# Performance work log

Measured on AMD Instinct MI355X. Metric: run time of the kernel, lower is better.

Reference implementation:

```python
import jax, jax.numpy as jnp
import numpy as np

B, S, D, H = 4, 2048, 1024, 16
HD = D // H
DFF = 4 * D
NUM_LAYERS = 12
RES = 1.0 / float(np.sqrt(NUM_LAYERS))
SCALE = 1.0 / float(np.sqrt(D))  # module divides by sqrt(embed_dim), not head_dim
EPS = 1e-5


def setup_inputs() -> dict:
    key = jax.random.key(0)
    ks = jax.random.split(key, 12)
    s = 0.02
    p = lambda k, shp: (jax.random.normal(k, shp, jnp.float32) * s)
    return {
        "x": jax.random.normal(ks[0], (B, S, D), jnp.float32),
        "Wq": p(ks[1], (D, D)), "bq": jnp.zeros((D,), jnp.float32),
        "Wk": p(ks[2], (D, D)), "bk": jnp.zeros((D,), jnp.float32),
        "Wv": p(ks[3], (D, D)), "bv": jnp.zeros((D,), jnp.float32),
        "Wo": p(ks[4], (D, D)), "bo": jnp.zeros((D,), jnp.float32),
        "g1": jnp.ones((D,), jnp.float32), "be1": jnp.zeros((D,), jnp.float32),
        "g2": jnp.ones((D,), jnp.float32), "be2": jnp.zeros((D,), jnp.float32),
        "W1": p(ks[5], (D, DFF)), "b1": jnp.zeros((DFF,), jnp.float32),
        "W2": p(ks[6], (DFF, D)), "b2": jnp.zeros((D,), jnp.float32),
    }


def _layernorm(x, g, b):
    m = jnp.mean(x, axis=-1, keepdims=True)
    v = jnp.mean((x - m) ** 2, axis=-1, keepdims=True)
    return (x - m) * jax.lax.rsqrt(v + EPS) * g + b


def _attention(x, Wq, bq, Wk, bk, Wv, bv, Wo, bo):
    b, s, d = x.shape
    q = (x @ Wq + bq).reshape(b, s, H, HD)
    k = (x @ Wk + bk).reshape(b, s, H, HD)
    v = (x @ Wv + bv).reshape(b, s, H, HD)
    scores = jnp.einsum('bqhd,bkhd->bhqk', q, k) * SCALE  # [B,H,S,S]
    mask = jnp.tril(jnp.ones((s, s), dtype=bool))
    scores = jnp.where(mask, scores, -jnp.inf)
    attn = jax.nn.softmax(scores, axis=-1)  # dropout_rate=0 -> identity
    out = jnp.einsum('bhqk,bkhd->bqhd', attn, v).reshape(b, s, d)
    return out @ Wo + bo


def reference(x, Wq, bq, Wk, bk, Wv, bv, Wo, bo, g1, be1, g2, be2, W1, b1, W2, b2):
    x = x + RES * _attention(_layernorm(x, g1, be1), Wq, bq, Wk, bk, Wv, bv, Wo, bo)
    h = _layernorm(x, g2, be2)
    ffn = jax.nn.relu(h @ W1 + b1) @ W2 + b2
    x = x + RES * ffn
    return x
```

## Files before the change

kernel.cpp:

```cpp
#include <hip/hip_runtime.h>

typedef unsigned short ushort_t;
typedef unsigned int uint32;
typedef __attribute__((ext_vector_type(4))) float f32x4;
typedef __attribute__((ext_vector_type(8))) short bf16x8;

#define B_   4
#define S_   2048
#define D_   1024
#define H_   16
#define HD_  64
#define DFF_ 4096
#define M_   (B_ * S_)

#define RES_   0.28867513459481287f
#define SCALE_ 0.03125f
#define EPS_   1e-5f
#define LOG2E_ 1.4426950408889634f

__device__ __forceinline__ ushort_t f2bf(float f) {
    union { float f; uint32 u; } c; c.f = f;
    uint32 u = c.u + 0x7fffu + ((c.u >> 16) & 1u);
    return (ushort_t)(u >> 16);
}
__device__ __forceinline__ float bf2f(ushort_t h) {
    union { uint32 u; float f; } c; c.u = ((uint32)h) << 16;
    return c.f;
}
__device__ __forceinline__ float fexp2(float x) {
    float r; asm("v_exp_f32 %0, %1" : "=v"(r) : "v"(x)); return r;
}
__device__ __forceinline__ uint32 cvt_pk_bf16(float lo, float hi) {
    uint32 r;
    asm("v_cvt_pk_bf16_f32 %0, %1, %2" : "=v"(r) : "v"(lo), "v"(hi));
    return r;
}

#define GLDS(src_, dst_)                                                     \
    __builtin_amdgcn_global_load_lds(                                        \
        (const __attribute__((address_space(1))) void*)(src_),               \
        (__attribute__((address_space(3))) void*)(dst_), 16, 0, 0)

__global__ __launch_bounds__(256) void transpose_cast_kernel(
    const float* __restrict__ W, ushort_t* __restrict__ Wt, int K, int N)
{
    __shared__ float tile[32][33];
    const int bx = blockIdx.x * 32;
    const int by = blockIdx.y * 32;
    const int tx = threadIdx.x;
    const int ty = threadIdx.y;
    #pragma unroll
    for (int i = 0; i < 32; i += 8)
        tile[ty + i][tx] = W[(size_t)(by + ty + i) * N + bx + tx];
    __syncthreads();
    #pragma unroll
    for (int i = 0; i < 32; i += 8)
        Wt[(size_t)(bx + ty + i) * K + by + tx] = f2bf(tile[tx][ty + i]);
}

__global__ void concat_bias_kernel(const float* __restrict__ bq,
                                   const float* __restrict__ bk,
                                   const float* __restrict__ bv,
                                   float* __restrict__ bqkv)
{
    int i = blockIdx.x * blockDim.x + threadIdx.x;
    if (i < 3 * D_) {
        float v = (i < D_) ? bq[i] : (i < 2 * D_) ? bk[i - D_] : bv[i - 2 * D_];
        bqkv[i] = v;
    }
}

__global__ __launch_bounds__(256) void ln_kernel(
    const float* __restrict__ x, const float* __restrict__ g,
    const float* __restrict__ be, ushort_t* __restrict__ out)
{
    const int row = blockIdx.x;
    const int t = threadIdx.x;
    const int lane = t & 63;
    const int wave = t >> 6;
    const float4* xr = (const float4*)(x + (size_t)row * D_);
    float4 v = xr[t];
    float s  = v.x + v.y + v.z + v.w;
    float s2 = v.x * v.x + v.y * v.y + v.z * v.z + v.w * v.w;
    #pragma unroll
    for (int off = 32; off; off >>= 1) {
        s  += __shfl_xor(s, off);
        s2 += __shfl_xor(s2, off);
    }
    __shared__ float red[8];
    if (lane == 0) { red[wave * 2] = s; red[wave * 2 + 1] = s2; }
    __syncthreads();
    s  = red[0] + red[2] + red[4] + red[6];
    s2 = red[1] + red[3] + red[5] + red[7];
    const float mean = s * (1.0f / D_);
    const float var  = s2 * (1.0f / D_) - mean * mean;
    const float rstd = rsqrtf(var + EPS_);
    const float4 gv  = ((const float4*)g)[t];
    const float4 bv  = ((const float4*)be)[t];
    ushort_t o[4];
    o[0] = f2bf((v.x - mean) * rstd * gv.x + bv.x);
    o[1] = f2bf((v.y - mean) * rstd * gv.y + bv.y);
    o[2] = f2bf((v.z - mean) * rstd * gv.z + bv.z);
    o[3] = f2bf((v.w - mean) * rstd * gv.w + bv.w);
    *(ushort2*)&out[(size_t)row * D_ + t * 4]     = make_ushort2(o[0], o[1]);
    *(ushort2*)&out[(size_t)row * D_ + t * 4 + 2] = make_ushort2(o[2], o[3]);
}

__global__ __launch_bounds__(256) void vtrans_kernel(
    const ushort_t* __restrict__ qkv, ushort_t* __restrict__ vt)
{
    __shared__ __align__(16) ushort_t T[256 * 64];
    const int tid  = threadIdx.x;
    const int sblk = blockIdx.x & 7;
    const int bh   = blockIdx.x >> 3;
    const int b = bh >> 4, h = bh & 15;
    const ushort_t* src = qkv + (size_t)(b * S_ + sblk * 256) * (3 * D_) + 2 * D_ + h * 64;
    #pragma unroll
    for (int p = 0; p < 8; ++p) {
        const int L = p * 256 + tid;
        const int s = L >> 3, c = L & 7;
        bf16x8 v = *(const bf16x8*)(src + (size_t)s * (3 * D_) + c * 8);
        *(bf16x8*)&T[s * 64 + ((c ^ (s & 7)) << 3)] = v;
    }
    __syncthreads();
    #pragma unroll
    for (int p = 0; p < 8; ++p) {
        const int L = p * 256 + tid;
        const int hd = L >> 5, scn = L & 31;
        ushort_t tmp[8];
        #pragma unroll
        for (int j = 0; j < 8; ++j) {
            const int s = scn * 8 + j;
            tmp[j] = T[s * 64 + (((hd >> 3) ^ (s & 7)) << 3) + (hd & 7)];
        }
        *(bf16x8*)&vt[((size_t)bh * 64 + hd) * S_ + sblk * 256 + scn * 8] =
            *(const bf16x8*)tmp;
    }
}

template <int MODE>
__global__ __launch_bounds__(512, 2) void gemmT_kernel(
    const ushort_t* __restrict__ A, const ushort_t* __restrict__ Bt,
    const float* __restrict__ bias, const float* __restrict__ res,
    void* __restrict__ Cout, int M, int N, int K, int gx)
{
    constexpr int LOADS = 3;

    __shared__ __align__(16) ushort_t As[3][128 * 32];
    __shared__ __align__(16) ushort_t Bs[3][256 * 32];

    const int tid  = threadIdx.x;
    const int w    = tid >> 6;
    const int lane = tid & 63;
    const int l15  = lane & 15;
    const int g    = lane >> 4;

    const int cpx = gridDim.x >> 3;
    const int swz = (blockIdx.x & 7) * cpx + (blockIdx.x >> 3);
    const int bx = swz % gx, by = swz / gx;
    const int m0 = by * 128, n0 = bx * 256;

    const int wm = (w >> 2) * 64;
    const int wn = (w & 3) * 64;

    const ushort_t* srcA;
    int ldsA;
    const ushort_t* srcB[2];
    int ldsB[2];
    {
        const int L = tid;
        const int row = L >> 2;
        srcA = A + (size_t)(m0 + row) * K + (((L & 3) ^ ((row >> 1) & 3)) << 3);
        ldsA = (w * 64) * 8;
    }
    #pragma unroll
    for (int p = 0; p < 2; ++p) {
        const int L = p * 512 + tid;
        const int row = L >> 2;
        srcB[p] = Bt + (size_t)(n0 + row) * K + (((L & 3) ^ ((row >> 1) & 3)) << 3);
        ldsB[p] = (p * 512 + w * 64) * 8;
    }

    #define STAGE(koff_, buf_)                                               \
        do {                                                                 \
            GLDS(srcA + (koff_), &As[buf_][ldsA]);                           \
            GLDS(srcB[0] + (koff_), &Bs[buf_][ldsB[0]]);                     \
            GLDS(srcB[1] + (koff_), &Bs[buf_][ldsB[1]]);                     \
        } while (0)

    #define LDA(mf_) (*(const bf16x8*)&As[cur][(wm + (mf_) * 16 + l15) * 32 + \
                        ((g ^ (((wm + (mf_) * 16 + l15) >> 1) & 3)) << 3)])
    #define LDB(nf_) (*(const bf16x8*)&Bs[cur][(wn + (nf_) * 16 + l15) * 32 + \
                        ((g ^ (((wn + (nf_) * 16 + l15) >> 1) & 3)) << 3)])

    f32x4 acc[4][4] = {};
    const int NT = K >> 5;

    STAGE(0, 0);
    STAGE(32, 1);
    asm volatile("s_waitcnt vmcnt(%0)" :: "n"(LOADS) : "memory");
    __builtin_amdgcn_s_barrier();

    for (int t = 0; t < NT; ++t) {
        const int cur = t % 3;
        const bool more = (t + 2 < NT);
        const size_t koff = (size_t)(t + 2) * 32;

        bf16x8 af[4], bfr[4];
        #pragma unroll
        for (int nf = 0; nf < 4; ++nf) bfr[nf] = LDB(nf);
        #pragma unroll
        for (int mf = 0; mf < 4; ++mf) af[mf] = LDA(mf);

        if (more) STAGE(koff, (t + 2) % 3);
        __builtin_amdgcn_s_setprio(1);
        #pragma unroll
        for (int mf = 0; mf < 4; ++mf)
            #pragma unroll
            for (int nf = 0; nf < 4; ++nf)
                acc[mf][nf] = __builtin_amdgcn_mfma_f32_16x16x32_bf16(
                    af[mf], bfr[nf], acc[mf][nf], 0, 0, 0);
        __builtin_amdgcn_s_setprio(0);
        if (more)
            asm volatile("s_waitcnt vmcnt(%0)" :: "n"(LOADS) : "memory");
        else
            asm volatile("s_waitcnt vmcnt(0)" ::: "memory");
        __builtin_amdgcn_s_barrier();
    }
    #undef STAGE
    #undef LDA
    #undef LDB

    const int rbase = g * 4;
    #pragma unroll
    for (int mf = 0; mf < 4; ++mf) {
        #pragma unroll
        for (int nf = 0; nf < 4; ++nf) {
            const int col = n0 + wn + nf * 16 + l15;
            const float bcol = bias[col];
            #pragma unroll
            for (int r = 0; r < 4; ++r) {
                const int row = m0 + wm + mf * 16 + rbase + r;
                float v = acc[mf][nf][r] + bcol;
                const size_t idx = (size_t)row * N + col;
                if (MODE == 0) {
                    ((ushort_t*)Cout)[idx] = f2bf(v);
                } else if (MODE == 1) {
                    ((ushort_t*)Cout)[idx] = f2bf(fmaxf(v, 0.0f));
                } else {
                    ((float*)Cout)[idx] = res[idx] + RES_ * v;
                }
            }
        }
    }
}

__global__ __launch_bounds__(256) void fattn_kernel(
    const ushort_t* __restrict__ qkv, const ushort_t* __restrict__ vtg,
    ushort_t* __restrict__ out)
{
    __shared__ __align__(16) ushort_t Ks[2][64 * 64];
    __shared__ __align__(16) ushort_t Vt[2][64 * 64];
    __shared__ __align__(16) ushort_t Ps[4][16 * 64];

    const int tid  = threadIdx.x;
    const int lane = tid & 63;
    const int w    = tid >> 6;
    const int lin  = blockIdx.x;
    const int xi   = lin >> 6;
    const int bh   = lin & 63;
    const int b = bh >> 4, h = bh & 15;

    const int l15 = lane & 15;
    const int g   = lane >> 4;

    const size_t rs = 3 * D_;
    const ushort_t* Qg = qkv + (size_t)b * S_ * rs + h * HD_;
    const ushort_t* Kg = Qg + D_;
    const ushort_t* Vg = vtg + (size_t)bh * HD_ * S_;

    const int srow = tid >> 3;
    const int sc   = tid & 7;

    #pragma unroll
    for (int half = 0; half < 2; ++half) {
        const int qt = half ? xi : (S_ / 64 - 1) - xi;
        const int q0 = qt * 64;
        const int nkb = qt + 1;

        bf16x8 qf[2];
        {
            const int qrow = q0 + w * 16 + l15;
            #pragma unroll
            for (int kk = 0; kk < 2; ++kk) {
                bf16x8 tq = *(const bf16x8*)(Qg + (size_t)qrow * rs + kk * 32 + g * 8);
                #pragma unroll
                for (int e = 0; e < 8; ++e)
                    tq[e] = (short)f2bf(bf2f((ushort_t)tq[e]) * (SCALE_ * LOG2E_));
                qf[kk] = tq;
            }
        }

        float mrow = -1e30f, lrow = 0.f;
        f32x4 oacc[4] = {};

        bf16x8 kvreg[2][2], vvreg[2][2];
        #pragma unroll
        for (int p = 0; p < 2; ++p) {
            const int row = p * 32 + srow;
            kvreg[0][p] = *(const bf16x8*)(Kg + (size_t)row * rs + sc * 8);
            vvreg[0][p] = *(const bf16x8*)(Vg + (size_t)row * S_ + sc * 8);
        }
        if (nkb > 1) {
            #pragma unroll
            for (int p = 0; p < 2; ++p) {
                const int row = p * 32 + srow;
                kvreg[1][p] = *(const bf16x8*)(Kg + (size_t)(64 + row) * rs + sc * 8);
                vvreg[1][p] = *(const bf16x8*)(Vg + (size_t)row * S_ + 64 + sc * 8);
            }
        }

        int kb = 0;
        for (; kb + 1 < nkb; kb += 2) {
            __syncthreads();
            #pragma unroll
            for (int s = 0; s < 2; ++s)
                #pragma unroll
                for (int p = 0; p < 2; ++p) {
                    const int row = p * 32 + srow;
                    *(bf16x8*)&Ks[s][row * 64 + ((sc ^ (row & 7)) << 3)] = kvreg[s][p];
                    *(bf16x8*)&Vt[s][row * 64 + ((sc ^ (row & 7)) << 3)] = vvreg[s][p];
                }
            if (kb + 2 < nkb) {
                #pragma unroll
                for (int p = 0; p < 2; ++p) {
                    const int row = p * 32 + srow;
                    kvreg[0][p] = *(const bf16x8*)(
                        Kg + (size_t)((kb + 2) * 64 + row) * rs + sc * 8);
                    vvreg[0][p] = *(const bf16x8*)(
                        Vg + (size_t)row * S_ + (kb + 2) * 64 + sc * 8);
                }
            }
            if (kb + 3 < nkb) {
                #pragma unroll
                for (int p = 0; p < 2; ++p) {
                    const int row = p * 32 + srow;
                    kvreg[1][p] = *(const bf16x8*)(
                        Kg + (size_t)((kb + 3) * 64 + row) * rs + sc * 8);
                    vvreg[1][p] = *(const bf16x8*)(
                        Vg + (size_t)row * S_ + (kb + 3) * 64 + sc * 8);
                }
            }
            __syncthreads();

            f32x4 sf0[4] = {}, sf1[4] = {};
            __builtin_amdgcn_s_setprio(1);
            #pragma unroll
            for (int kk = 0; kk < 2; ++kk) {
                const int cc = kk * 4 + g;
                #pragma unroll
                for (int nf = 0; nf < 4; ++nf) {
                    const int keyr = nf * 16 + l15;
                    const int ko = keyr * 64 + ((cc ^ (keyr & 7)) << 3);
                    bf16x8 kf0 = *(const bf16x8*)&Ks[0][ko];
                    bf16x8 kf1 = *(const bf16x8*)&Ks[1][ko];
                    sf0[nf] = __builtin_amdgcn_mfma_f32_16x16x32_bf16(kf0, qf[kk], sf0[nf], 0, 0, 0);
                    sf1[nf] = __builtin_amdgcn_mfma_f32_16x16x32_bf16(kf1, qf[kk], sf1[nf], 0, 0, 0);
                }
            }
            __builtin_amdgcn_s_setprio(0);

            if (kb + 1 == nkb - 1) {
                const int q = q0 + w * 16 + l15;
                #pragma unroll
                for (int nf = 0; nf < 4; ++nf)
                    #pragma unroll
                    for (int r = 0; r < 4; ++r)
                        if ((kb + 1) * 64 + nf * 16 + g * 4 + r > q) sf1[nf][r] = -1e30f;
            }

            float mx = -1e30f;
            #pragma unroll
            for (int nf = 0; nf < 4; ++nf)
                #pragma unroll
                for (int r = 0; r < 4; ++r) {
                    mx = fmaxf(mx, sf0[nf][r]);
                    mx = fmaxf(mx, sf1[nf][r]);
                }
            mx = fmaxf(mx, __shfl_xor(mx, 16));
            mx = fmaxf(mx, __shfl_xor(mx, 32));

            if (!__all(mx - mrow <= 8.0f)) {
                const float mnew = fmaxf(mrow, mx);
                const float corr = fexp2(mrow - mnew);
                mrow = mnew;
                lrow *= corr;
                #pragma unroll
                for (int r = 0; r < 4; ++r) {
                    const float cr = __shfl(corr, g * 4 + r, 16);
                    #pragma unroll
                    for (int nf = 0; nf < 4; ++nf) oacc[nf][r] *= cr;
                }
            }

            float psum = 0.f;
            const int qrow = l15;
            #pragma unroll
            for (int s = 0; s < 2; ++s) {
                const f32x4* sfp = s ? sf1 : sf0;
                #pragma unroll
                for (int nf = 0; nf < 4; ++nf) {
                    const float p0 = fexp2(sfp[nf][0] - mrow);
                    const float p1 = fexp2(sfp[nf][1] - mrow);
                    const float p2 = fexp2(sfp[nf][2] - mrow);
                    const float p3 = fexp2(sfp[nf][3] - mrow);
                    psum += (p0 + p1) + (p2 + p3);
                    uint2 pk = make_uint2(cvt_pk_bf16(p0, p1), cvt_pk_bf16(p2, p3));
                    const int c16 = ((nf << 1) + (g >> 1)) ^ (qrow & 7);
                    *(uint2*)((char*)Ps[w] + qrow * 128 + c16 * 16 + (g & 1) * 8) = pk;
                }
                #pragma unroll
                for (int kk = 0; kk < 2; ++kk) {
                    const int cc = kk * 4 + g;
                    const int c16 = cc ^ (qrow & 7);
                    bf16x8 pa = *(const bf16x8*)((const char*)Ps[w] + qrow * 128 + c16 * 16);
                    __builtin_amdgcn_s_setprio(1);
                    #pragma unroll
                    for (int nf = 0; nf < 4; ++nf) {
                        const int dr = nf * 16 + l15;
                        bf16x8 vf = *(const bf16x8*)&Vt[s][dr * 64 + ((cc ^ (dr & 7)) << 3)];
                        oacc[nf] = __builtin_amdgcn_mfma_f32_16x16x32_bf16(pa, vf, oacc[nf], 0, 0, 0);
                    }
                    __builtin_amdgcn_s_setprio(0);
                }
            }
            psum += __shfl_xor(psum, 16);
            psum += __shfl_xor(psum, 32);
            lrow += psum;
        }

        if (kb < nkb) {
            __syncthreads();
            #pragma unroll
            for (int p = 0; p < 2; ++p) {
                const int row = p * 32 + srow;
                *(bf16x8*)&Ks[0][row * 64 + ((sc ^ (row & 7)) << 3)] = kvreg[0][p];
                *(bf16x8*)&Vt[0][row * 64 + ((sc ^ (row & 7)) << 3)] = vvreg[0][p];
            }
            __syncthreads();

            f32x4 sf0[4] = {};
            __builtin_amdgcn_s_setprio(1);
            #pragma unroll
            for (int kk = 0; kk < 2; ++kk) {
                const int cc = kk * 4 + g;
                #pragma unroll
                for (int nf = 0; nf < 4; ++nf) {
                    const int keyr = nf * 16 + l15;
                    bf16x8 kf = *(const bf16x8*)&Ks[0][keyr * 64 + ((cc ^ (keyr & 7)) << 3)];
                    sf0[nf] = __builtin_amdgcn_mfma_f32_16x16x32_bf16(kf, qf[kk], sf0[nf], 0, 0, 0);
                }
            }
            __builtin_amdgcn_s_setprio(0);

            {
                const int q = q0 + w * 16 + l15;
                #pragma unroll
                for (int nf = 0; nf < 4; ++nf)
                    #pragma unroll
                    for (int r = 0; r < 4; ++r)
                        if (kb * 64 + nf * 16 + g * 4 + r > q) sf0[nf][r] = -1e30f;
            }
            float mx = -1e30f;
            #pragma unroll
            for (int nf = 0; nf < 4; ++nf)
                #pragma unroll
                for (int r = 0; r < 4; ++r) mx = fmaxf(mx, sf0[nf][r]);
            mx = fmaxf(mx, __shfl_xor(mx, 16));
            mx = fmaxf(mx, __shfl_xor(mx, 32));

            if (!__all(mx - mrow <= 8.0f)) {
                const float mnew = fmaxf(mrow, mx);
                const float corr = fexp2(mrow - mnew);
                mrow = mnew;
                lrow *= corr;
                #pragma unroll
                for (int r = 0; r < 4; ++r) {
                    const float cr = __shfl(corr, g * 4 + r, 16);
                    #pragma unroll
                    for (int nf = 0; nf < 4; ++nf) oacc[nf][r] *= cr;
                }
            }

            float psum = 0.f;
            const int qrow = l15;
            #pragma unroll
            for (int nf = 0; nf < 4; ++nf) {
                const float p0 = fexp2(sf0[nf][0] - mrow);
                const float p1 = fexp2(sf0[nf][1] - mrow);
                const float p2 = fexp2(sf0[nf][2] - mrow);
                const float p3 = fexp2(sf0[nf][3] - mrow);
                psum += (p0 + p1) + (p2 + p3);
                uint2 pk = make_uint2(cvt_pk_bf16(p0, p1), cvt_pk_bf16(p2, p3));
                const int c16 = ((nf << 1) + (g >> 1)) ^ (qrow & 7);
                *(uint2*)((char*)Ps[w] + qrow * 128 + c16 * 16 + (g & 1) * 8) = pk;
            }
            psum += __shfl_xor(psum, 16);
            psum += __shfl_xor(psum, 32);
            lrow += psum;

            #pragma unroll
            for (int kk = 0; kk < 2; ++kk) {
                const int cc = kk * 4 + g;
                const int c16 = cc ^ (qrow & 7);
                bf16x8 pa = *(const bf16x8*)((const char*)Ps[w] + qrow * 128 + c16 * 16);
                __builtin_amdgcn_s_setprio(1);
                #pragma unroll
                for (int nf = 0; nf < 4; ++nf) {
                    const int dr = nf * 16 + l15;
                    bf16x8 vf = *(const bf16x8*)&Vt[0][dr * 64 + ((cc ^ (dr & 7)) << 3)];
                    oacc[nf] = __builtin_amdgcn_mfma_f32_16x16x32_bf16(pa, vf, oacc[nf], 0, 0, 0);
                }
                __builtin_amdgcn_s_setprio(0);
            }
        }

        const float linv = 1.0f / lrow;
        #pragma unroll
        for (int r = 0; r < 4; ++r) {
            const float li = __shfl(linv, g * 4 + r, 16);
            const int q = q0 + w * 16 + g * 4 + r;
            ushort_t* op = out + (size_t)(b * S_ + q) * D_ + h * HD_;
            #pragma unroll
            for (int nf = 0; nf < 4; ++nf)
                op[nf * 16 + l15] = f2bf(oacc[nf][r] * li);
        }
    }
}

extern "C" void kernel_launch(void* const* d_in, const int* in_sizes, int n_in,
                              void* d_out, int out_size, void* d_ws, size_t ws_size,
                              hipStream_t stream)
{
    const float* x   = (const float*)d_in[0];
    const float* Wq  = (const float*)d_in[1];
    const float* bq  = (const float*)d_in[2];
    const float* Wk  = (const float*)d_in[3];
    const float* bk  = (const float*)d_in[4];
    const float* Wv  = (const float*)d_in[5];
    const float* bv  = (const float*)d_in[6];
    const float* Wo  = (const float*)d_in[7];
    const float* bo  = (const float*)d_in[8];
    const float* g1  = (const float*)d_in[9];
    const float* be1 = (const float*)d_in[10];
    const float* g2  = (const float*)d_in[11];
    const float* be2 = (const float*)d_in[12];
    const float* W1  = (const float*)d_in[13];
    const float* b1  = (const float*)d_in[14];
    const float* W2  = (const float*)d_in[15];
    const float* b2  = (const float*)d_in[16];
    float* out = (float*)d_out;

    char* ws = (char*)d_ws;
    size_t o = 0;
    auto alloc = [&](size_t bytes) { size_t r = o; o = (o + bytes + 255) & ~(size_t)255; return r; };
    ushort_t* Wqkvt = (ushort_t*)(ws + alloc((size_t)3 * D_ * D_ * 2));
    ushort_t* Wot   = (ushort_t*)(ws + alloc((size_t)D_ * D_ * 2));
    ushort_t* W1t   = (ushort_t*)(ws + alloc((size_t)DFF_ * D_ * 2));
    ushort_t* W2t   = (ushort_t*)(ws + alloc((size_t)D_ * DFF_ * 2));
    float*    bqkv  = (float*)(ws + alloc((size_t)3 * D_ * 4));
    ushort_t* lnbuf = (ushort_t*)(ws + alloc((size_t)M_ * D_ * 2));
    ushort_t* bigbuf= (ushort_t*)(ws + alloc((size_t)M_ * DFF_ * 2));
    ushort_t* attnb = (ushort_t*)(ws + alloc((size_t)M_ * D_ * 2));
    float*    x1    = (float*)(ws + alloc((size_t)M_ * D_ * 4));
    ushort_t* vtbuf = (ushort_t*)(ws + alloc((size_t)M_ * D_ * 2));

    dim3 tblock(32, 8);
    transpose_cast_kernel<<<dim3(D_/32, D_/32), tblock, 0, stream>>>(Wq, Wqkvt,            D_, D_);
    transpose_cast_kernel<<<dim3(D_/32, D_/32), tblock, 0, stream>>>(Wk, Wqkvt + D_*D_,    D_, D_);
    transpose_cast_kernel<<<dim3(D_/32, D_/32), tblock, 0, stream>>>(Wv, Wqkvt + 2*D_*D_,  D_, D_);
    transpose_cast_kernel<<<dim3(D_/32, D_/32), tblock, 0, stream>>>(Wo, Wot,              D_, D_);
    transpose_cast_kernel<<<dim3(DFF_/32, D_/32), tblock, 0, stream>>>(W1, W1t,            D_, DFF_);
    transpose_cast_kernel<<<dim3(D_/32, DFF_/32), tblock, 0, stream>>>(W2, W2t,            DFF_, D_);
    concat_bias_kernel<<<12, 256, 0, stream>>>(bq, bk, bv, bqkv);

    ln_kernel<<<M_, 256, 0, stream>>>(x, g1, be1, lnbuf);
    gemmT_kernel<0><<<(M_/128)*(3*D_/256), 512, 0, stream>>>(
        lnbuf, Wqkvt, bqkv, nullptr, bigbuf, M_, 3*D_, D_, 3*D_/256);
    vtrans_kernel<<<512, 256, 0, stream>>>(bigbuf, vtbuf);
    fattn_kernel<<<(S_/128) * 64, 256, 0, stream>>>(bigbuf, vtbuf, attnb);
    gemmT_kernel<2><<<(M_/128)*(D_/256), 512, 0, stream>>>(
        attnb, Wot, bo, x, x1, M_, D_, D_, D_/256);
    ln_kernel<<<M_, 256, 0, stream>>>(x1, g2, be2, lnbuf);
    gemmT_kernel<1><<<(M_/128)*(DFF_/256), 512, 0, stream>>>(
        lnbuf, W1t, b1, nullptr, bigbuf, M_, DFF_, D_, DFF_/256);
    gemmT_kernel<2><<<(M_/128)*(D_/256), 512, 0, stream>>>(
        bigbuf, W2t, b2, x1, out, M_, D_, DFF_, D_/256);
}
```

Baseline: 381.4 us.

## Add 256x256-tile ping-pong GEMM kernel for QKV and FFN1 projections

Result: no change. 386.2 us (+1.2%).

```diff
diff --git a/kernel.cpp b/kernel.cpp
--- a/kernel.cpp
+++ b/kernel.cpp
@@ -135,6 +135,146 @@
         }
         *(bf16x8*)&vt[((size_t)bh * 64 + hd) * S_ + sblk * 256 + scn * 8] =
             *(const bf16x8*)tmp;
+    }
+}
+
+template <int MODE>
+__global__ __launch_bounds__(512, 1) void gemm8p_kernel(
+    const ushort_t* __restrict__ A, const ushort_t* __restrict__ Bt,
+    const float* __restrict__ bias, const float* __restrict__ res,
+    void* __restrict__ Cout, int M, int N, int K, int gx)
+{
+    __shared__ __align__(16) ushort_t As[2][256 * 64];
+    __shared__ __align__(16) ushort_t Bs[2][256 * 64];
+
+    const int tid  = threadIdx.x;
+    const int w    = tid >> 6;
+    const int lane = tid & 63;
+    const int l15  = lane & 15;
+    const int g    = lane >> 4;
+
+    const int cpx = gridDim.x >> 3;
+    const int swz = (blockIdx.x & 7) * cpx + (blockIdx.x >> 3);
+    const int bx = swz % gx, by = swz / gx;
+    const int m0 = by * 256, n0 = bx * 256;
+
+    const int wm = (w >> 2) * 128;
+    const int wn = (w & 3) * 64;
+
+    const ushort_t* srcA[4];
+    const ushort_t* srcB[4];
+    int ldsO[4];
+    #pragma unroll
+    for (int p = 0; p < 4; ++p) {
+        const int L = p * 512 + tid;
+        const int row = L >> 3;
+        const int c = ((L & 7) ^ (row & 7)) << 3;
+        srcA[p] = A  + (size_t)(m0 + row) * K + c;
+        srcB[p] = Bt + (size_t)(n0 + row) * K + c;
+        ldsO[p] = (p * 512 + w * 64) * 8;
+    }
+
+    #define LDA(mf_, kk_) (*(const bf16x8*)&As[cur][(wm + (mf_) * 16 + l15) * 64 + \
+                  (((((kk_) * 4 + g)) ^ ((wm + (mf_) * 16 + l15) & 7)) << 3)])
+    #define LDB(nf_, kk_) (*(const bf16x8*)&Bs[cur][(wn + (nf_) * 16 + l15) * 64 + \
+                  (((((kk_) * 4 + g)) ^ ((wn + (nf_) * 16 + l15) & 7)) << 3)])
+    #define MM4(base_)                                                         \
+        do { _Pragma("unroll")                                                 \
+             for (int mf = 0; mf < 4; ++mf)                                    \
+                 _Pragma("unroll")                                             \
+                 for (int nf = 0; nf < 4; ++nf)                                \
+                     acc[(base_) + mf][nf] =                                   \
+                         __builtin_amdgcn_mfma_f32_16x16x32_bf16(              \
+                             af[mf], bfr[nf], acc[(base_) + mf][nf], 0, 0, 0); \
+        } while (0)
+
+    f32x4 acc[8][4] = {};
+    const int NT = K >> 6;
+
+    #pragma unroll
+    for (int p = 0; p < 4; ++p) GLDS(srcA[p], &As[0][ldsO[p]]);
+    #pragma unroll
+    for (int p = 0; p < 4; ++p) GLDS(srcB[p], &Bs[0][ldsO[p]]);
+    asm volatile("s_waitcnt vmcnt(0)" ::: "memory");
+    __builtin_amdgcn_s_barrier();
+
+    for (int t = 0; t < NT; ++t) {
+        const int cur = t & 1;
+        const int nb  = cur ^ 1;
+        const bool more = (t + 1 < NT);
+        const size_t koff = (size_t)(t + 1) * 64;
+
+        bf16x8 af[4], bfr[4];
+
+        #pragma unroll
+        for (int nf = 0; nf < 4; ++nf) bfr[nf] = LDB(nf, 0);
+        #pragma unroll
+        for (int mf = 0; mf < 4; ++mf) af[mf] = LDA(mf, 0);
+        if (more) {
+            #pragma unroll
+            for (int p = 0; p < 4; ++p) GLDS(srcA[p] + koff, &As[nb][ldsO[p]]);
+        }
+        __builtin_amdgcn_s_barrier();
+        __builtin_amdgcn_s_setprio(1);
+        MM4(0);
+        __builtin_amdgcn_s_setprio(0);
+        __builtin_amdgcn_s_barrier();
+
+        #pragma unroll
+        for (int mf = 0; mf < 4; ++mf) af[mf] = LDA(mf + 4, 0);
+        if (more) {
+            #pragma unroll
+            for (int p = 0; p < 4; ++p) GLDS(srcB[p] + koff, &Bs[nb][ldsO[p]]);
+        }
+        __builtin_amdgcn_s_barrier();
+        __builtin_amdgcn_s_setprio(1);
+        MM4(4);
+        __builtin_amdgcn_s_setprio(0);
+        __builtin_amdgcn_s_barrier();
+
+        #pragma unroll
+        for (int nf = 0; nf < 4; ++nf) bfr[nf] = LDB(nf, 1);
+        #pragma unroll
+        for (int mf = 0; mf < 4; ++mf) af[mf] = LDA(mf, 1);
+        __builtin_amdgcn_s_barrier();
+        __builtin_amdgcn_s_setprio(1);
+        MM4(0);
+        __builtin_amdgcn_s_setprio(0);
+        __builtin_amdgcn_s_barrier();
+
+        #pragma unroll
+        for (int mf = 0; mf < 4; ++mf) af[mf] = LDA(mf + 4, 1);
+        __builtin_amdgcn_s_setprio(1);
+        MM4(4);
+        __builtin_amdgcn_s_setprio(0);
+        asm volatile("s_waitcnt vmcnt(0)" ::: "memory");
+        __builtin_amdgcn_s_barrier();
+    }
+    #undef LDA
+    #undef LDB
+    #undef MM4
+
+    const int rbase = g * 4;
+    #pragma unroll
+    for (int mf = 0; mf < 8; ++mf) {
+        #pragma unroll
+        for (int nf = 0; nf < 4; ++nf) {
+            const int col = n0 + wn + nf * 16 + l15;
+            const float bcol = bias[col];
+            #pragma unroll
+            for (int r = 0; r < 4; ++r) {
+                const int row = m0 + wm + mf * 16 + rbase + r;
+                float v = acc[mf][nf][r] + bcol;
+                const size_t idx = (size_t)row * N + col;
+                if (MODE == 0) {
+                    ((ushort_t*)Cout)[idx] = f2bf(v);
+                } else if (MODE == 1) {
+                    ((ushort_t*)Cout)[idx] = f2bf(fmaxf(v, 0.0f));
+                } else {
+                    ((float*)Cout)[idx] = res[idx] + RES_ * v;
+                }
+            }
+        }
     }
 }
 
@@ -585,14 +725,14 @@
     concat_bias_kernel<<<12, 256, 0, stream>>>(bq, bk, bv, bqkv);
 
     ln_kernel<<<M_, 256, 0, stream>>>(x, g1, be1, lnbuf);
-    gemmT_kernel<0><<<(M_/128)*(3*D_/256), 512, 0, stream>>>(
+    gemm8p_kernel<0><<<(M_/256)*(3*D_/256), 512, 0, stream>>>(
         lnbuf, Wqkvt, bqkv, nullptr, bigbuf, M_, 3*D_, D_, 3*D_/256);
     vtrans_kernel<<<512, 256, 0, stream>>>(bigbuf, vtbuf);
     fattn_kernel<<<(S_/128) * 64, 256, 0, stream>>>(bigbuf, vtbuf, attnb);
     gemmT_kernel<2><<<(M_/128)*(D_/256), 512, 0, stream>>>(
         attnb, Wot, bo, x, x1, M_, D_, D_, D_/256);
     ln_kernel<<<M_, 256, 0, stream>>>(x1, g2, be2, lnbuf);
-    gemmT_kernel<1><<<(M_/128)*(DFF_/256), 512, 0, stream>>>(
+    gemm8p_kernel<1><<<(M_/256)*(DFF_/256), 512, 0, stream>>>(
         lnbuf, W1t, b1, nullptr, bigbuf, M_, DFF_, D_, DFF_/256);
     gemmT_kernel<2><<<(M_/128)*(D_/256), 512, 0, stream>>>(
         bigbuf, W2t, b2, x1, out, M_, D_, DFF_, D_/256);
```
